# Optimization experiments

Hardware: AMD Instinct MI355X
Metric: run time of the kernel (lower is better)

Reference implementation:

```python
import jax, jax.numpy as jnp
import numpy as np

B, C, T, H, Wd = 8, 256, 16, 28, 28

def setup_inputs() -> dict:
    key = jax.random.key(0)
    k1, k2 = jax.random.split(key)
    in_data = jax.random.normal(k1, (B, C, T, H, Wd), dtype=jnp.float32)
    # conv_whh weight [C, C, 1, 1, 1] squeezed to [C_out, C_in]; scaled like kaiming init
    W = jax.random.normal(k2, (C, C), dtype=jnp.float32) * (1.0 / jnp.sqrt(jnp.float32(C)))
    return {"in_data": in_data, "W": W}

def reference(in_data, W):
    # h_0 = x_0; h_t = (W @ h_{t-1} + x_t) / 2, out = stack over t
    x0 = in_data[:, :, 0]                      # [B, C, H, W]
    xs = jnp.moveaxis(in_data[:, :, 1:], 2, 0) # [T-1, B, C, H, W]

    def step(h, x_t):
        h_new = (jnp.einsum('oc,bchw->bohw', W, h) + x_t) * 0.5
        return h_new, h_new

    _, outs = jax.lax.scan(step, x0, xs)       # [T-1, B, C, H, W]
    out = jnp.concatenate([x0[None], outs], axis=0)  # [T, B, C, H, W]
    return jnp.moveaxis(out, 0, 2)             # [B, C, T, H, W]
```

## Files before the change

### kernel.cpp

```cpp
#include <hip/hip_runtime.h>
#include <hip/hip_bf16.h>


typedef __attribute__((ext_vector_type(8))) short bf16x8;
typedef __attribute__((ext_vector_type(4))) float f32x4;

#define NTILES 49
#define LDSK   264
#define CSTRIDE 12544

#define AS1 __attribute__((address_space(1)))
#define AS3 __attribute__((address_space(3)))

__device__ __forceinline__ void ld_lds16(const float* g, float* l) {
    __builtin_amdgcn_global_load_lds((AS1 const unsigned int*)g,
                                     (AS3 unsigned int*)l, 16, 0, 0);
}

__device__ __forceinline__ int pkbf2(float a, float b) {
    __hip_bfloat162 h = __float22bfloat162_rn(make_float2(a, b));
    union { __hip_bfloat162 h2; int i; } u; u.h2 = h; return u.i;
}

__device__ __forceinline__ short f2bf(float f) {
    union { float f; unsigned u; } v; v.f = f;
    unsigned r = v.u + 0x7FFFu + ((v.u >> 16) & 1u);
    return (short)(r >> 16);
}

__global__ __launch_bounds__(256, 2)
void rcu_kernel(const float* __restrict__ in, const float* __restrict__ Wm,
                float* __restrict__ out) {
    __shared__ short hbuf[2][16][LDSK];
    __shared__ float xslab[256 * 16];

    const int tid  = threadIdx.x;
    const int wave = tid >> 6;
    const int lane = tid & 63;
    const int l15  = lane & 15;
    const int quad = lane >> 4;

    const int b  = blockIdx.x / NTILES;
    const int s0 = (blockIdx.x % NTILES) * 16;

    const size_t base = (size_t)b * 256 * CSTRIDE + s0;
    const float* xin  = in  + base;
    float*       xout = out + base;

    const int pf_c   = lane >> 2;
    const int pf_col = (lane & 3) * 4;

#pragma unroll
    for (int i = 0; i < 4; ++i) {
        const int cb = wave * 64 + i * 16;
        ld_lds16(xin + (size_t)(cb + pf_c) * CSTRIDE + pf_col,
                 &xslab[cb * 16]);
    }

    bf16x8 a_frag[4][8];
#pragma unroll
    for (int mt = 0; mt < 4; ++mt) {
        const int m = wave * 64 + mt * 16 + l15;
        const float* wrow = Wm + m * 256 + quad * 8;
#pragma unroll
        for (int ks = 0; ks < 8; ++ks) {
            float4 f0 = *(const float4*)(wrow + ks * 32);
            float4 f1 = *(const float4*)(wrow + ks * 32 + 4);
            bf16x8 a;
            a[0] = f2bf(f0.x); a[1] = f2bf(f0.y); a[2] = f2bf(f0.z); a[3] = f2bf(f0.w);
            a[4] = f2bf(f1.x); a[5] = f2bf(f1.y); a[6] = f2bf(f1.z); a[7] = f2bf(f1.w);
            a_frag[mt][ks] = a;
        }
    }

    __asm__ volatile("s_waitcnt vmcnt(0)" ::: "memory");
#pragma unroll
    for (int mt = 0; mt < 4; ++mt) {
        const int c0 = wave * 64 + mt * 16 + quad * 4;
        float v[4];
#pragma unroll
        for (int r = 0; r < 4; ++r) {
            v[r] = xslab[(c0 + r) * 16 + l15];
            xout[(size_t)(c0 + r) * CSTRIDE + l15] = v[r];
        }
        int2 packed;
        packed.x = pkbf2(v[0], v[1]);
        packed.y = pkbf2(v[2], v[3]);
        *(int2*)&hbuf[0][l15][c0] = packed;
    }
    __asm__ volatile("s_waitcnt lgkmcnt(0)\n\ts_barrier" ::: "memory");

    int cur = 0;
    int tof = 784;
#pragma unroll 1
    for (int t = 1; t < 16; ++t) {
#pragma unroll
        for (int i = 0; i < 4; ++i) {
            const int cb = wave * 64 + i * 16;
            ld_lds16(xin + (size_t)(cb + pf_c) * CSTRIDE + tof + pf_col,
                     &xslab[cb * 16]);
        }

        bf16x8 bfrag[8];
        const short* hp = &hbuf[cur][l15][quad * 8];
#pragma unroll
        for (int ks = 0; ks < 8; ++ks)
            bfrag[ks] = *(const bf16x8*)(hp + ks * 32);

        f32x4 acc[4];
#pragma unroll
        for (int mt = 0; mt < 4; ++mt) {
            f32x4 a0 = {0.f, 0.f, 0.f, 0.f};
#pragma unroll
            for (int ks = 0; ks < 8; ++ks)
                a0 = __builtin_amdgcn_mfma_f32_16x16x32_bf16(a_frag[mt][ks], bfrag[ks], a0, 0, 0, 0);
            acc[mt] = a0;
        }

        __asm__ volatile("s_waitcnt vmcnt(0)" ::: "memory");

        const int nxt = cur ^ 1;
#pragma unroll
        for (int mt = 0; mt < 4; ++mt) {
            const int c0 = wave * 64 + mt * 16 + quad * 4;
            float v[4];
#pragma unroll
            for (int r = 0; r < 4; ++r) {
                v[r] = 0.5f * (acc[mt][r] + xslab[(c0 + r) * 16 + l15]);
                xout[(size_t)(c0 + r) * CSTRIDE + tof + l15] = v[r];
            }
            int2 packed;
            packed.x = pkbf2(v[0], v[1]);
            packed.y = pkbf2(v[2], v[3]);
            *(int2*)&hbuf[nxt][l15][c0] = packed;
        }

        __asm__ volatile("s_waitcnt lgkmcnt(0)\n\ts_barrier" ::: "memory");

        tof += 784;
        cur = nxt;
    }
}

extern "C" void kernel_launch(void* const* d_in, const int* in_sizes, int n_in,
                              void* d_out, int out_size, void* d_ws, size_t ws_size,
                              hipStream_t stream) {
    const float* in  = (const float*)d_in[0];
    const float* Wm  = (const float*)d_in[1];
    float*       out = (float*)d_out;
    hipLaunchKernelGGL(rcu_kernel, dim3(8 * NTILES), dim3(256), 0, stream, in, Wm, out);
}
```

Baseline: 232.0 us.

## Triple-buffer input slabs and prefetch two timesteps ahead with partial vmcnt wait

Expands the LDS x slab into a three-deep ring buffer so each timestep's input is fetched two iterations ahead. The full vmcnt(0) wait becomes vmcnt(40), so the pending global stores and the newer prefetches can stay in flight while the current slab is consumed. The W loads are also issued as a batch before the x prefetches and the bf16 conversion, which overlaps the load latencies. In exchange it uses more LDS (possibly lowering occupancy), does some redundant clamped loads on the last steps, and depends on a hand-counted vmcnt threshold being exact.

```diff
diff --git a/kernel.cpp b/kernel.cpp
--- a/kernel.cpp
+++ b/kernel.cpp
@@ -32,7 +32,7 @@
 void rcu_kernel(const float* __restrict__ in, const float* __restrict__ Wm,
                 float* __restrict__ out) {
     __shared__ short hbuf[2][16][LDSK];
-    __shared__ float xslab[256 * 16];
+    __shared__ float xslab[3][256 * 16];
 
     const int tid  = threadIdx.x;
     const int wave = tid >> 6;
@@ -50,37 +50,46 @@
     const int pf_c   = lane >> 2;
     const int pf_col = (lane & 3) * 4;
 
-#pragma unroll
-    for (int i = 0; i < 4; ++i) {
-        const int cb = wave * 64 + i * 16;
-        ld_lds16(xin + (size_t)(cb + pf_c) * CSTRIDE + pf_col,
-                 &xslab[cb * 16]);
-    }
-
     bf16x8 a_frag[4][8];
+    float4 wtmp[4][8][2];
 #pragma unroll
     for (int mt = 0; mt < 4; ++mt) {
         const int m = wave * 64 + mt * 16 + l15;
         const float* wrow = Wm + m * 256 + quad * 8;
 #pragma unroll
         for (int ks = 0; ks < 8; ++ks) {
-            float4 f0 = *(const float4*)(wrow + ks * 32);
-            float4 f1 = *(const float4*)(wrow + ks * 32 + 4);
+            wtmp[mt][ks][0] = *(const float4*)(wrow + ks * 32);
+            wtmp[mt][ks][1] = *(const float4*)(wrow + ks * 32 + 4);
+        }
+    }
+#pragma unroll
+    for (int s = 0; s < 3; ++s)
+#pragma unroll
+        for (int i = 0; i < 4; ++i) {
+            const int cb = wave * 64 + i * 16;
+            ld_lds16(xin + (size_t)(cb + pf_c) * CSTRIDE + s * 784 + pf_col,
+                     &xslab[s][cb * 16]);
+        }
+#pragma unroll
+    for (int mt = 0; mt < 4; ++mt)
+#pragma unroll
+        for (int ks = 0; ks < 8; ++ks) {
+            float4 f0 = wtmp[mt][ks][0], f1 = wtmp[mt][ks][1];
             bf16x8 a;
             a[0] = f2bf(f0.x); a[1] = f2bf(f0.y); a[2] = f2bf(f0.z); a[3] = f2bf(f0.w);
             a[4] = f2bf(f1.x); a[5] = f2bf(f1.y); a[6] = f2bf(f1.z); a[7] = f2bf(f1.w);
             a_frag[mt][ks] = a;
         }
-    }
 
     __asm__ volatile("s_waitcnt vmcnt(0)" ::: "memory");
+
 #pragma unroll
     for (int mt = 0; mt < 4; ++mt) {
         const int c0 = wave * 64 + mt * 16 + quad * 4;
         float v[4];
 #pragma unroll
         for (int r = 0; r < 4; ++r) {
-            v[r] = xslab[(c0 + r) * 16 + l15];
+            v[r] = xslab[0][(c0 + r) * 16 + l15];
             xout[(size_t)(c0 + r) * CSTRIDE + l15] = v[r];
         }
         int2 packed;
@@ -90,15 +99,19 @@
     }
     __asm__ volatile("s_waitcnt lgkmcnt(0)\n\ts_barrier" ::: "memory");
 
+    float* sp = xslab[0];
+    float* sc = xslab[1];
+    float* sn = xslab[2];
     int cur = 0;
     int tof = 784;
 #pragma unroll 1
     for (int t = 1; t < 16; ++t) {
+        const int tpf = (t + 2 <= 15) ? (t + 2) * 784 : 15 * 784;
 #pragma unroll
         for (int i = 0; i < 4; ++i) {
             const int cb = wave * 64 + i * 16;
-            ld_lds16(xin + (size_t)(cb + pf_c) * CSTRIDE + tof + pf_col,
-                     &xslab[cb * 16]);
+            ld_lds16(xin + (size_t)(cb + pf_c) * CSTRIDE + tpf + pf_col,
+                     sp + cb * 16);
         }
 
         bf16x8 bfrag[8];
@@ -117,7 +130,7 @@
             acc[mt] = a0;
         }
 
-        __asm__ volatile("s_waitcnt vmcnt(0)" ::: "memory");
+        __asm__ volatile("s_waitcnt vmcnt(40)" ::: "memory");
 
         const int nxt = cur ^ 1;
 #pragma unroll
@@ -126,7 +139,7 @@
             float v[4];
 #pragma unroll
             for (int r = 0; r < 4; ++r) {
-                v[r] = 0.5f * (acc[mt][r] + xslab[(c0 + r) * 16 + l15]);
+                v[r] = 0.5f * (acc[mt][r] + sc[(c0 + r) * 16 + l15]);
                 xout[(size_t)(c0 + r) * CSTRIDE + tof + l15] = v[r];
             }
             int2 packed;
@@ -137,6 +150,7 @@
 
         __asm__ volatile("s_waitcnt lgkmcnt(0)\n\ts_barrier" ::: "memory");
 
+        float* tmp = sp; sp = sc; sc = sn; sn = tmp;
         tof += 784;
         cur = nxt;
     }
```

Measured after the change: 248.3 us. 7.0% more time.
